# Performance work log

Measured on AMD Instinct MI355X. Metric: run time of the kernel, lower is better.

The kernel has to match this reference:

```python
import jax, jax.numpy as jnp
import numpy as np

VAT_TOKENS = 57
ACTION_NUM = 56
NUM_HEADS = 16
DIM = 1152
HEAD_DIM = DIM // NUM_HEADS
SCALE = HEAD_DIM ** -0.5
N_GROUPS = 3  # num_non_act = 768 -> 3 groups of 256


def setup_inputs() -> dict:
    key = jax.random.key(0)
    ks = jax.random.split(key, 8)
    B, N, C = 32, VAT_TOKENS + 768, DIM
    w_std = C ** -0.5
    return {
        "x": jax.random.normal(ks[0], (B, N, C), jnp.float32),
        "w_qkv_non": jax.random.normal(ks[1], (3 * C, C), jnp.float32) * w_std,
        "w_q_act": jax.random.normal(ks[2], (C, C), jnp.float32) * w_std,
        "w_kv_act": jax.random.normal(ks[3], (2 * C, C), jnp.float32) * w_std,
        "w_proj_non": jax.random.normal(ks[4], (C, C), jnp.float32) * w_std,
        "b_proj_non": jnp.zeros((C,), jnp.float32),
        "w_proj_act": jax.random.normal(ks[5], (C, C), jnp.float32) * w_std,
        "b_proj_act": jnp.zeros((C,), jnp.float32),
    }


def reference(x, w_qkv_non, w_q_act, w_kv_act, w_proj_non, b_proj_non,
              w_proj_act, b_proj_act):
    B, N, C = x.shape
    H, Dh = NUM_HEADS, HEAD_DIM
    num_non_act = N - VAT_TOKENS
    G = num_non_act // N_GROUPS  # group size (256)

    # ---- non-action stream: windowed (grouped) self-attention ----
    non_act = x[:, VAT_TOKENS:]                                  # (B, 768, C)
    qkv = non_act @ w_qkv_non.T                                  # (B, 768, 3C)
    qkv = qkv.reshape(B, N_GROUPS, G, 3, H, Dh)
    q = qkv[:, :, :, 0]                                          # (B, g, G, H, Dh)
    k = qkv[:, :, :, 1]
    v = qkv[:, :, :, 2]
    attn = jnp.einsum('bgqhd,bgkhd->bghqk', q, k) * SCALE
    attn = jax.nn.softmax(attn, axis=-1)
    x_non = jnp.einsum('bghqk,bgkhd->bgqhd', attn, v)
    x_non = x_non.reshape(B, num_non_act, C)

    # ---- action stream: act queries attend to x[ACTION_NUM:] ----
    act = x[:, :VAT_TOKENS]
    q_act = (act @ w_q_act.T).reshape(B, VAT_TOKENS, H, Dh)
    kv = (x @ w_kv_act.T).reshape(B, N, 2, H, Dh)
    k_act = kv[:, ACTION_NUM:, 0]                                # (B, N-56, H, Dh)
    v_act = kv[:, ACTION_NUM:, 1]
    attn_act = jnp.einsum('bqhd,bkhd->bhqk', q_act, k_act) * SCALE
    attn_act = jax.nn.softmax(attn_act, axis=-1)
    x_act = jnp.einsum('bhqk,bkhd->bqhd', attn_act, v_act)
    x_act = x_act.reshape(B, VAT_TOKENS, C)

    # ---- output projections + concat ----
    x_non = x_non @ w_proj_non.T + b_proj_non
    x_act = x_act @ w_proj_act.T + b_proj_act
    return jnp.concatenate([x_act, x_non], axis=1)
```

## Files before the change

kernel.cpp:

```cpp
#include <hip/hip_runtime.h>

typedef __attribute__((ext_vector_type(8))) __bf16 bf16x8;
typedef __attribute__((ext_vector_type(4))) float f32x4;
typedef __attribute__((ext_vector_type(4))) unsigned short u16x4;
typedef __attribute__((ext_vector_type(8))) unsigned short u16x8;

#define MFMA_BF16 __builtin_amdgcn_mfma_f32_16x16x32_bf16

__device__ __forceinline__ unsigned short f2bf(float f) {
  union { float f; unsigned u; } v; v.f = f;
  unsigned r = v.u + 0x7FFFu + ((v.u >> 16) & 1u);
  return (unsigned short)(r >> 16);
}

__device__ __forceinline__ void gload16(const void* g, void* l) {
  __builtin_amdgcn_global_load_lds(
      (const __attribute__((address_space(1))) unsigned int*)g,
      (__attribute__((address_space(3))) unsigned int*)l, 16, 0, 0);
}

__device__ __forceinline__ void cast8(const float* __restrict__ in,
                                      unsigned short* __restrict__ out, long i) {
  long base = i * 8;
  float4 a = *(const float4*)(in + base);
  float4 b = *(const float4*)(in + base + 4);
  u16x8 o;
  o[0] = f2bf(a.x); o[1] = f2bf(a.y); o[2] = f2bf(a.z); o[3] = f2bf(a.w);
  o[4] = f2bf(b.x); o[5] = f2bf(b.y); o[6] = f2bf(b.z); o[7] = f2bf(b.w);
  *(u16x8*)(out + base) = o;
}

__global__ void __launch_bounds__(256) cast_all(
    const float* __restrict__ x, const float* __restrict__ wqkv,
    const float* __restrict__ wq, const float* __restrict__ wkv,
    const float* __restrict__ wpn, const float* __restrict__ wpa,
    unsigned short* __restrict__ xb, unsigned short* __restrict__ wqkvb,
    unsigned short* __restrict__ wqb, unsigned short* __restrict__ wkvb,
    unsigned short* __restrict__ wpnb, unsigned short* __restrict__ wpab) {
  const long c0 = 3801600, c1 = 4299264, c2 = 4465152, c3 = 4796928,
             c4 = 4962816, c5 = 5128704;
  long i = (long)blockIdx.x * 256 + threadIdx.x;
  if (i >= c5) return;
  if (i < c0)      cast8(x,    xb,    i);
  else if (i < c1) cast8(wqkv, wqkvb, i - c0);
  else if (i < c2) cast8(wq,   wqb,   i - c1);
  else if (i < c3) cast8(wkv,  wkvb,  i - c2);
  else if (i < c4) cast8(wpn,  wpnb,  i - c3);
  else             cast8(wpa,  wpab,  i - c4);
}

template <int REMAP>
__device__ __forceinline__ long remap_row(int m) {
  if (REMAP == 1) { int b = m / 768; return (long)b * 825 + 57 + (m - b * 768); }
  if (REMAP == 2) { int b = m / 57;  return (long)b * 825 + (m - b * 57); }
  return m;
}

template <int REMAP, bool PROJ>
__device__ __forceinline__ void gemm_body(unsigned short* L, int orig, int gx, int nwg,
                                          const unsigned short* __restrict__ A,
                                          const unsigned short* __restrict__ Bw,
                                          void* __restrict__ Cout,
                                          const float* __restrict__ bias,
                                          int M, int N) {
  const int K = 1152;
  unsigned short* Al = L;
  unsigned short* Bl = L + 32768;
  int tid = threadIdx.x;
  int lane = tid & 63;
  int wid = tid >> 6;
  int l15 = lane & 15, hi = lane >> 4;
  int wm = wid >> 2, wn = wid & 3;

  int q8 = nwg >> 3, r8 = nwg & 7;
  int xcd = orig & 7, off = orig >> 3;
  int wgid = (xcd < r8 ? xcd * (q8 + 1) : r8 * (q8 + 1) + (xcd - r8) * q8) + off;
  int bn = wgid % gx, bm = wgid / gx;
  int m0 = bm * 256, n0 = bn * 256;

  int rlo = tid >> 2;
  int cg = ((tid & 3) - (tid >> 3)) & 3;
  int ma0 = m0 + rlo;       if (ma0 > M - 1) ma0 = M - 1;
  int ma1 = m0 + rlo + 128; if (ma1 > M - 1) ma1 = M - 1;
  const unsigned short* aptr0 = A + remap_row<REMAP>(ma0) * K + cg * 8;
  const unsigned short* aptr1 = A + remap_row<REMAP>(ma1) * K + cg * 8;
  int nb0 = n0 + rlo;       if (nb0 > N - 1) nb0 = N - 1;
  int nb1 = n0 + rlo + 128; if (nb1 > N - 1) nb1 = N - 1;
  const unsigned short* bptr0 = Bw + (long)nb0 * K + cg * 8;
  const unsigned short* bptr1 = Bw + (long)nb1 * K + cg * 8;
  unsigned ldst = (unsigned)tid * 8;

  unsigned short* Ad = Al + ldst;
  unsigned short* Bd = Bl + ldst;

  const int cl = (hi + (l15 >> 1)) & 3;
  const unsigned short* arb[4];
  const unsigned short* brb[4];
#pragma unroll
  for (int f = 0; f < 4; ++f) {
    arb[f] = Al + (wm * 128 + f * 16 + l15) * 32 + cl * 8;
    brb[f] = Bl + (wn * 64 + f * 16 + l15) * 32 + cl * 8;
  }

#define STAGE(P)                                                        \
  {                                                                     \
    gload16(aptr0 + (P) * 32, Ad + (((P) & 3) << 13));                  \
    gload16(aptr1 + (P) * 32, Ad + ((((P) & 3) << 13)) + 4096);         \
    gload16(bptr0 + (P) * 32, Bd + (((P) & 3) << 13));                  \
    gload16(bptr1 + (P) * 32, Bd + ((((P) & 3) << 13)) + 4096);         \
  }
#define READ_FA(P, S)                                                   \
  {                                                                     \
    _Pragma("unroll") for (int f = 0; f < 8; ++f)                       \
        fA[S][f] = *(const bf16x8*)(arb[f & 3] + (((P) & 3) << 13) + (f >> 2) * 2048); \
  }
#define READ_FB(P)                                                      \
  {                                                                     \
    _Pragma("unroll") for (int f = 0; f < 4; ++f)                       \
        fB[f] = *(const bf16x8*)(brb[f] + (((P) & 3) << 13));           \
  }

  STAGE(0); STAGE(1); STAGE(2);
  __builtin_amdgcn_sched_barrier(0);
  asm volatile("s_waitcnt vmcnt(4)" ::: "memory");
  __builtin_amdgcn_s_barrier();
  __builtin_amdgcn_sched_barrier(0);

  bf16x8 fA[2][8];
  bf16x8 fB[4];
  READ_FA(0, 0);
  READ_FB(0);
  f32x4 acc[8][4] = {};

#pragma unroll
  for (int p = 0; p < 36; ++p) {
    const int cur = p & 1;
    if (p < 35) READ_FA(p + 1, cur ^ 1);
    __builtin_amdgcn_sched_barrier(0);
    __builtin_amdgcn_s_setprio(1);
#pragma unroll
    for (int fm = 0; fm < 8; ++fm)
#pragma unroll
      for (int fn = 0; fn < 4; ++fn)
        acc[fm][fn] = MFMA_BF16(fA[cur][fm], fB[fn], acc[fm][fn], 0, 0, 0);
    __builtin_amdgcn_s_setprio(0);
    if (p < 35) READ_FB(p + 1);
    if (p <= 32) STAGE(p + 3);
    if (p <= 32)      asm volatile("s_waitcnt vmcnt(4)" ::: "memory");
    else if (p == 33) asm volatile("s_waitcnt vmcnt(0)" ::: "memory");
    if (p < 35) {
      __builtin_amdgcn_sched_barrier(0);
      __builtin_amdgcn_s_barrier();
      __builtin_amdgcn_sched_barrier(0);
    }
  }
#undef STAGE
#undef READ_FA
#undef READ_FB

  if (!PROJ) {
    unsigned short* reg = L + wid * 8192;
#pragma unroll
    for (int a = 0; a < 8; ++a) {
#pragma unroll
      for (int fn = 0; fn < 4; ++fn) {
        int rbase = a * 16 + hi * 4;
#pragma unroll
        for (int r = 0; r < 4; ++r) {
          int row = rbase + r;
          int ch = (fn * 2 + (l15 >> 3)) ^ (row & 7);
          reg[row * 64 + ch * 8 + (l15 & 7)] = f2bf(acc[a][fn][r]);
        }
      }
    }
#pragma unroll
    for (int i = 0; i < 16; ++i) {
      int rr = i * 8 + (lane >> 3);
      int ch = (lane & 7) ^ (rr & 7);
      u16x8 v = *(const u16x8*)(reg + rr * 64 + ch * 8);
      int m = m0 + wm * 128 + rr;
      int n = n0 + wn * 64 + (lane & 7) * 8;
      if (m < M && n < N)
        *(u16x8*)((unsigned short*)Cout + (long)m * N + n) = v;
    }
  } else {
    float* regf = (float*)L + wid * 4096;
    float bv[4];
#pragma unroll
    for (int fn = 0; fn < 4; ++fn) {
      int n = n0 + wn * 64 + fn * 16 + l15;
      bv[fn] = bias[n < N ? n : N - 1];
    }
#pragma unroll
    for (int half = 0; half < 2; ++half) {
#pragma unroll
      for (int a4 = 0; a4 < 4; ++a4) {
#pragma unroll
        for (int fn = 0; fn < 4; ++fn) {
          int rbase = a4 * 16 + hi * 4;
#pragma unroll
          for (int r = 0; r < 4; ++r)
            regf[(rbase + r) * 64 + fn * 16 + l15] = acc[half * 4 + a4][fn][r] + bv[fn];
        }
      }
#pragma unroll
      for (int i = 0; i < 16; ++i) {
        int rr = i * 4 + (lane >> 4);
        int cc = (lane & 15) * 4;
        f32x4 v = *(const f32x4*)(regf + rr * 64 + cc);
        int m = m0 + wm * 128 + half * 64 + rr;
        int n = n0 + wn * 64 + cc;
        if (m < M && n < N)
          *(f32x4*)((float*)Cout + remap_row<REMAP>(m) * N + n) = v;
      }
      if (half == 0) asm volatile("s_waitcnt lgkmcnt(0)" ::: "memory");
    }
  }
}

__global__ void __launch_bounds__(512, 2) gemm_front(
    const unsigned short* __restrict__ xb, const unsigned short* __restrict__ wqkvb,
    const unsigned short* __restrict__ wkvb, const unsigned short* __restrict__ wqb,
    unsigned short* __restrict__ qkvw, unsigned short* __restrict__ kvw,
    unsigned short* __restrict__ qw) {
  __shared__ unsigned short L[65536];
  int bid = blockIdx.x;
  if (bid < 1344)
    gemm_body<1, false>(L, bid, 14, 1344, xb, wqkvb, qkvw, nullptr, 24576, 3456);
  else if (bid < 2280)
    gemm_body<0, false>(L, bid - 1344, 9, 936, xb, wkvb, kvw, nullptr, 26400, 2304);
  else
    gemm_body<2, false>(L, bid - 2280, 5, 40, xb, wqb, qw, nullptr, 1824, 1152);
}

__global__ void __launch_bounds__(512, 2) gemm_proj(
    const unsigned short* __restrict__ attnw, const unsigned short* __restrict__ wpnb,
    const unsigned short* __restrict__ wpab, float* __restrict__ out,
    const float* __restrict__ bpn, const float* __restrict__ bpa) {
  __shared__ unsigned short L[65536];
  int bid = blockIdx.x;
  if (bid < 480)
    gemm_body<1, true>(L, bid, 5, 480, attnw, wpnb, out, bpn, 24576, 1152);
  else
    gemm_body<2, true>(L, bid - 480, 5, 40, attnw, wpab, out, bpa, 1824, 1152);
}

__global__ void __launch_bounds__(256) attn_non(const unsigned short* __restrict__ qkv,
                                                unsigned short* __restrict__ o) {
  int h = blockIdx.x, g = blockIdx.y, b = blockIdx.z;
  __shared__ unsigned short K_s[128 * 104];
  __shared__ unsigned short V_s[80 * 136];
  __shared__ unsigned short P_s[16 * 16 * 40];
  int tid = threadIdx.x, lane = tid & 63, wid = tid >> 6;
  int l15 = lane & 15, hi = lane >> 4;
  const long base = (long)((b * 3 + g) * 256) * 3456;
  const float SC2 = 0.11785113019775793f * 1.4426950408889634f;

  bf16x8 qf[4][3];
#pragma unroll
  for (int qt = 0; qt < 4; qt++)
#pragma unroll
    for (int ds = 0; ds < 3; ds++) {
      int q = wid * 64 + qt * 16 + l15;
      int d = ds * 32 + hi * 8;
      if (d < 72)
        qf[qt][ds] = *(const bf16x8*)(qkv + base + (long)q * 3456 + h * 72 + d);
      else {
        u16x8 z = {0, 0, 0, 0, 0, 0, 0, 0};
        qf[qt][ds] = __builtin_bit_cast(bf16x8, z);
      }
    }

  f32x4 ot[5][4] = {};
  float lsum[4] = {0.f, 0.f, 0.f, 0.f};

  for (int c0 = 0; c0 < 256; c0 += 128) {
    {
      int r = tid >> 1, hf = tid & 1;
      const unsigned short* src = qkv + base + (long)(c0 + r) * 3456 + (16 + h) * 72 + hf * 48;
      unsigned short* dst = &K_s[r * 104 + hf * 48];
#pragma unroll
      for (int j = 0; j < 6; j++) {
        int col = hf * 48 + j * 8;
        u16x8 v = {0, 0, 0, 0, 0, 0, 0, 0};
        if (col < 72) v = *(const u16x8*)(src + j * 8);
        *(u16x8*)(dst + j * 8) = v;
      }
    }
    if (tid < 128) {
      const unsigned short* src = qkv + base + (long)(c0 + tid) * 3456 + (32 + h) * 72;
      u16x8 w[9];
#pragma unroll
      for (int j = 0; j < 9; j++) w[j] = *(const u16x8*)(src + j * 8);
#pragma unroll
      for (int j = 0; j < 9; j++)
#pragma unroll
        for (int e = 0; e < 8; e++) V_s[(j * 8 + e) * 136 + tid] = w[j][e];
    }
    __syncthreads();

#pragma unroll
    for (int k32 = 0; k32 < 4; k32++) {
#pragma unroll
      for (int kt = 0; kt < 2; kt++) {
        bf16x8 kf[3];
#pragma unroll
        for (int ds = 0; ds < 3; ds++)
          kf[ds] = *(const bf16x8*)((const char*)K_s +
                     ((k32 * 32 + kt * 16 + l15) * 104 + ds * 32 + hi * 8) * 2);
#pragma unroll
        for (int qt = 0; qt < 4; qt++) {
          f32x4 st = {};
#pragma unroll
          for (int ds = 0; ds < 3; ds++) st = MFMA_BF16(kf[ds], qf[qt][ds], st, 0, 0, 0);
          u16x4 pw;
#pragma unroll
          for (int r = 0; r < 4; r++) {
            float p = exp2f(st[r] * SC2);
            lsum[qt] += p;
            pw[r] = f2bf(p);
          }
          *(u16x4*)&P_s[((wid * 4 + qt) * 16 + l15) * 40 + kt * 16 + hi * 4] = pw;
        }
      }
      bf16x8 pf[4];
#pragma unroll
      for (int qt = 0; qt < 4; qt++)
        pf[qt] = *(const bf16x8*)&P_s[((wid * 4 + qt) * 16 + l15) * 40 + hi * 8];
#pragma unroll
      for (int dt = 0; dt < 5; dt++) {
        bf16x8 vf = *(const bf16x8*)&V_s[(dt * 16 + l15) * 136 + k32 * 32 + hi * 8];
#pragma unroll
        for (int qt = 0; qt < 4; qt++) ot[dt][qt] = MFMA_BF16(vf, pf[qt], ot[dt][qt], 0, 0, 0);
      }
    }
    __syncthreads();
  }

#pragma unroll
  for (int qt = 0; qt < 4; qt++) {
    float s = lsum[qt];
    s += __shfl_xor(s, 16);
    s += __shfl_xor(s, 32);
    lsum[qt] = 1.0f / s;
  }
#pragma unroll
  for (int dt = 0; dt < 5; dt++)
#pragma unroll
    for (int qt = 0; qt < 4; qt++)
#pragma unroll
      for (int r = 0; r < 4; r++) {
        int d = dt * 16 + hi * 4 + r;
        if (d < 72) {
          long row = (long)b * 825 + 57 + g * 256 + wid * 64 + qt * 16 + l15;
          o[row * 1152 + h * 72 + d] = f2bf(ot[dt][qt][r] * lsum[qt]);
        }
      }
}

__global__ void __launch_bounds__(256) attn_act(const unsigned short* __restrict__ kv,
                                                const unsigned short* __restrict__ qa,
                                                unsigned short* __restrict__ o) {
  int h = blockIdx.x, b = blockIdx.y;
  __shared__ unsigned short K_s[128 * 104];
  __shared__ unsigned short V_s[80 * 136];
  __shared__ unsigned short P_s[4 * 16 * 40];
  int tid = threadIdx.x, lane = tid & 63, wid = tid >> 6;
  int l15 = lane & 15, hi = lane >> 4;
  const float SC2 = 0.11785113019775793f * 1.4426950408889634f;
  const int LIM = 769;

  bf16x8 qf[3];
  {
    int q = wid * 16 + l15; if (q > 56) q = 56;
#pragma unroll
    for (int ds = 0; ds < 3; ds++) {
      int d = ds * 32 + hi * 8;
      if (d < 72)
        qf[ds] = *(const bf16x8*)(qa + (long)(b * 57 + q) * 1152 + h * 72 + d);
      else {
        u16x8 z = {0, 0, 0, 0, 0, 0, 0, 0};
        qf[ds] = __builtin_bit_cast(bf16x8, z);
      }
    }
  }

  f32x4 ot[5] = {};
  float lsum = 0.f;
  const long kbase = (long)b * 825 + 56;

  for (int c0 = 0; c0 < LIM; c0 += 128) {
    int valid = LIM - c0; if (valid > 128) valid = 128;
    {
      int r = tid >> 1, hf = tid & 1;
      int rr = r < valid ? r : valid - 1;
      const unsigned short* src = kv + (kbase + c0 + rr) * 2304 + h * 72 + hf * 48;
      unsigned short* dst = &K_s[r * 104 + hf * 48];
#pragma unroll
      for (int j = 0; j < 6; j++) {
        int col = hf * 48 + j * 8;
        u16x8 v = {0, 0, 0, 0, 0, 0, 0, 0};
        if (col < 72) v = *(const u16x8*)(src + j * 8);
        *(u16x8*)(dst + j * 8) = v;
      }
    }
    if (tid < 128) {
      int rr = tid < valid ? tid : valid - 1;
      const unsigned short* src = kv + (kbase + c0 + rr) * 2304 + (16 + h) * 72;
      u16x8 w[9];
#pragma unroll
      for (int j = 0; j < 9; j++) w[j] = *(const u16x8*)(src + j * 8);
#pragma unroll
      for (int j = 0; j < 9; j++)
#pragma unroll
        for (int e = 0; e < 8; e++) V_s[(j * 8 + e) * 136 + tid] = w[j][e];
    }
    __syncthreads();

#pragma unroll
    for (int k32 = 0; k32 < 4; k32++) {
#pragma unroll
      for (int kt = 0; kt < 2; kt++) {
        bf16x8 kf[3];
#pragma unroll
        for (int ds = 0; ds < 3; ds++)
          kf[ds] = *(const bf16x8*)((const char*)K_s +
                     ((k32 * 32 + kt * 16 + l15) * 104 + ds * 32 + hi * 8) * 2);
        f32x4 st = {};
#pragma unroll
        for (int ds = 0; ds < 3; ds++) st = MFMA_BF16(kf[ds], qf[ds], st, 0, 0, 0);
        u16x4 pw;
#pragma unroll
        for (int r = 0; r < 4; r++) {
          int kg = c0 + k32 * 32 + kt * 16 + hi * 4 + r;
          float p = (kg < LIM) ? exp2f(st[r] * SC2) : 0.f;
          lsum += p;
          pw[r] = f2bf(p);
        }
        *(u16x4*)&P_s[(wid * 16 + l15) * 40 + kt * 16 + hi * 4] = pw;
      }
      bf16x8 pf = *(const bf16x8*)&P_s[(wid * 16 + l15) * 40 + hi * 8];
#pragma unroll
      for (int dt = 0; dt < 5; dt++) {
        bf16x8 vf = *(const bf16x8*)&V_s[(dt * 16 + l15) * 136 + k32 * 32 + hi * 8];
        ot[dt] = MFMA_BF16(vf, pf, ot[dt], 0, 0, 0);
      }
    }
    __syncthreads();
  }

  {
    float s = lsum;
    s += __shfl_xor(s, 16);
    s += __shfl_xor(s, 32);
    lsum = 1.0f / s;
  }
  int q = wid * 16 + l15;
#pragma unroll
  for (int dt = 0; dt < 5; dt++)
#pragma unroll
    for (int r = 0; r < 4; r++) {
      int d = dt * 16 + hi * 4 + r;
      if (d < 72 && q < 57)
        o[((long)b * 825 + q) * 1152 + h * 72 + d] = f2bf(ot[dt][r] * lsum);
    }
}

extern "C" void kernel_launch(void* const* d_in, const int* in_sizes, int n_in,
                              void* d_out, int out_size, void* d_ws, size_t ws_size,
                              hipStream_t stream) {
  const float* x     = (const float*)d_in[0];
  const float* w_qkv = (const float*)d_in[1];
  const float* w_q   = (const float*)d_in[2];
  const float* w_kv  = (const float*)d_in[3];
  const float* w_pn  = (const float*)d_in[4];
  const float* b_pn  = (const float*)d_in[5];
  const float* w_pa  = (const float*)d_in[6];
  const float* b_pa  = (const float*)d_in[7];

  char* ws = (char*)d_ws;
  unsigned short* xb    = (unsigned short*)ws; ws += (size_t)26400 * 1152 * 2;
  unsigned short* wqkvb = (unsigned short*)ws; ws += (size_t)3456 * 1152 * 2;
  unsigned short* wqb   = (unsigned short*)ws; ws += (size_t)1152 * 1152 * 2;
  unsigned short* wkvb  = (unsigned short*)ws; ws += (size_t)2304 * 1152 * 2;
  unsigned short* wpnb  = (unsigned short*)ws; ws += (size_t)1152 * 1152 * 2;
  unsigned short* wpab  = (unsigned short*)ws; ws += (size_t)1152 * 1152 * 2;
  unsigned short* qkvw  = (unsigned short*)ws; ws += (size_t)24576 * 3456 * 2;
  unsigned short* kvw   = (unsigned short*)ws; ws += (size_t)26400 * 2304 * 2;
  unsigned short* qw    = (unsigned short*)ws; ws += (size_t)1824 * 1152 * 2;
  unsigned short* attnw = (unsigned short*)ws; ws += (size_t)26400 * 1152 * 2;

  cast_all<<<20034, 256, 0, stream>>>(x, w_qkv, w_q, w_kv, w_pn, w_pa,
                                      xb, wqkvb, wqb, wkvb, wpnb, wpab);

  gemm_front<<<2320, 512, 0, stream>>>(xb, wqkvb, wkvb, wqb, qkvw, kvw, qw);

  attn_non<<<dim3(16, 3, 32), 256, 0, stream>>>(qkvw, attnw);
  attn_act<<<dim3(16, 32), 256, 0, stream>>>(kvw, qw, attnw);

  gemm_proj<<<520, 512, 0, stream>>>(attnw, wpnb, wpab, (float*)d_out, b_pn, b_pa);
}
```

Baseline: 672.0 us.

## Issue next-stage loads earlier, merge attention kernels, reorder proj blocks

The GEMM main loop now issues the global-to-LDS stage load for step p+3 at the top of each iteration, before the fragment reads and MFMAs, so memory latency has more time to overlap compute. The two attention kernels are merged into one launch, with the action stream as an extra grid-y slice. This removes a launch and lets the action heads run alongside the non-action groups. The projection kernel dispatches the small action GEMM blocks first so they do not trail at the tail. Issuing the stage load earlier may write into an LDS buffer still being read unless the ring depth covers it, and the merged kernel allocates the larger P_s for every block.

```diff
diff --git a/kernel.cpp b/kernel.cpp
--- a/kernel.cpp
+++ b/kernel.cpp
@@ -135,6 +135,7 @@
 #pragma unroll
   for (int p = 0; p < 36; ++p) {
     const int cur = p & 1;
+    if (p <= 32) STAGE(p + 3);
     if (p < 35) READ_FA(p + 1, cur ^ 1);
     __builtin_amdgcn_sched_barrier(0);
     __builtin_amdgcn_s_setprio(1);
@@ -145,7 +146,6 @@
         acc[fm][fn] = MFMA_BF16(fA[cur][fm], fB[fn], acc[fm][fn], 0, 0, 0);
     __builtin_amdgcn_s_setprio(0);
     if (p < 35) READ_FB(p + 1);
-    if (p <= 32) STAGE(p + 3);
     if (p <= 32)      asm volatile("s_waitcnt vmcnt(4)" ::: "memory");
     else if (p == 33) asm volatile("s_waitcnt vmcnt(0)" ::: "memory");
     if (p < 35) {
@@ -239,18 +239,17 @@
     const float* __restrict__ bpn, const float* __restrict__ bpa) {
   __shared__ unsigned short L[65536];
   int bid = blockIdx.x;
-  if (bid < 480)
-    gemm_body<1, true>(L, bid, 5, 480, attnw, wpnb, out, bpn, 24576, 1152);
+  if (bid < 40)
+    gemm_body<2, true>(L, bid, 5, 40, attnw, wpab, out, bpa, 1824, 1152);
   else
-    gemm_body<2, true>(L, bid - 480, 5, 40, attnw, wpab, out, bpa, 1824, 1152);
-}
-
-__global__ void __launch_bounds__(256) attn_non(const unsigned short* __restrict__ qkv,
-                                                unsigned short* __restrict__ o) {
-  int h = blockIdx.x, g = blockIdx.y, b = blockIdx.z;
-  __shared__ unsigned short K_s[128 * 104];
-  __shared__ unsigned short V_s[80 * 136];
-  __shared__ unsigned short P_s[16 * 16 * 40];
+    gemm_body<1, true>(L, bid - 40, 5, 480, attnw, wpnb, out, bpn, 24576, 1152);
+}
+
+__device__ __forceinline__ void attn_non_body(unsigned short* K_s, unsigned short* V_s,
+                                              unsigned short* P_s,
+                                              const unsigned short* __restrict__ qkv,
+                                              unsigned short* __restrict__ o,
+                                              int h, int g, int b) {
   int tid = threadIdx.x, lane = tid & 63, wid = tid >> 6;
   int l15 = lane & 15, hi = lane >> 4;
   const long base = (long)((b * 3 + g) * 256) * 3456;
@@ -358,13 +357,12 @@
       }
 }
 
-__global__ void __launch_bounds__(256) attn_act(const unsigned short* __restrict__ kv,
-                                                const unsigned short* __restrict__ qa,
-                                                unsigned short* __restrict__ o) {
-  int h = blockIdx.x, b = blockIdx.y;
-  __shared__ unsigned short K_s[128 * 104];
-  __shared__ unsigned short V_s[80 * 136];
-  __shared__ unsigned short P_s[4 * 16 * 40];
+__device__ __forceinline__ void attn_act_body(unsigned short* K_s, unsigned short* V_s,
+                                              unsigned short* P_s,
+                                              const unsigned short* __restrict__ kv,
+                                              const unsigned short* __restrict__ qa,
+                                              unsigned short* __restrict__ o,
+                                              int h, int b) {
   int tid = threadIdx.x, lane = tid & 63, wid = tid >> 6;
   int l15 = lane & 15, hi = lane >> 4;
   const float SC2 = 0.11785113019775793f * 1.4426950408889634f;
@@ -464,6 +462,20 @@
       if (d < 72 && q < 57)
         o[((long)b * 825 + q) * 1152 + h * 72 + d] = f2bf(ot[dt][r] * lsum);
     }
+}
+
+__global__ void __launch_bounds__(256) attn_all(const unsigned short* __restrict__ qkv,
+                                                const unsigned short* __restrict__ kv,
+                                                const unsigned short* __restrict__ qa,
+                                                unsigned short* __restrict__ o) {
+  __shared__ unsigned short K_s[128 * 104];
+  __shared__ unsigned short V_s[80 * 136];
+  __shared__ unsigned short P_s[16 * 16 * 40];
+  int h = blockIdx.x, y = blockIdx.y, b = blockIdx.z;
+  if (y < 3)
+    attn_non_body(K_s, V_s, P_s, qkv, o, h, y, b);
+  else
+    attn_act_body(K_s, V_s, P_s, kv, qa, o, h, b);
 }
 
 extern "C" void kernel_launch(void* const* d_in, const int* in_sizes, int n_in,
@@ -495,8 +507,7 @@
 
   gemm_front<<<2320, 512, 0, stream>>>(xb, wqkvb, wkvb, wqb, qkvw, kvw, qw);
 
-  attn_non<<<dim3(16, 3, 32), 256, 0, stream>>>(qkvw, attnw);
-  attn_act<<<dim3(16, 32), 256, 0, stream>>>(kvw, qw, attnw);
+  attn_all<<<dim3(16, 4, 32), 256, 0, stream>>>(qkvw, kvw, qw, attnw);
 
   gemm_proj<<<520, 512, 0, stream>>>(attnw, wpnb, wpab, (float*)d_out, b_pn, b_pa);
 }
```

Measured after the change: 696.1 us. 3.6% more time.
